# Optimization experiments

Measured on AMD Instinct MI355X. Metric: run time of the kernel, lower is better.

The kernel has to match this reference:

```python
import jax, jax.numpy as jnp
import numpy as np

N_NODES = 50000
N_EDGES = 800000
N_GRAPHS = 32
D = 300
NUM_CLASSES = 40


def setup_inputs() -> dict:
    key = jax.random.key(0)
    ks = jax.random.split(key, 32)

    def w(k, shape):
        fan_in = shape[-2]
        return (jax.random.normal(k, shape, jnp.float32) / np.sqrt(fan_in)).astype(jnp.float32)

    inp = {
        'x': jax.random.normal(ks[0], (N_NODES, 3), jnp.float32),
        'edge_index': jax.random.randint(ks[1], (2, N_EDGES), 0, N_NODES, jnp.int32),
        'batch': jnp.sort(jax.random.randint(ks[2], (N_NODES,), 0, N_GRAPHS, jnp.int32)),
        # project MLP [3, 64, 128, 300]
        'pW1': w(ks[3], (3, 64)),   'pb1': jnp.zeros((64,), jnp.float32),
        'pW2': w(ks[4], (64, 128)), 'pb2': jnp.zeros((128,), jnp.float32),
        'pW3': w(ks[5], (128, D)),  'pb3': jnp.zeros((D,), jnp.float32),
        # 3 PointGNNConv layers, params stacked on leading axis
        'hW': w(ks[6], (3, D, 3)),      'hb': jnp.zeros((3, 3), jnp.float32),
        'fW': w(ks[7], (3, D + 3, D)),  'fb': jnp.zeros((3, D), jnp.float32),
        'gW': w(ks[8], (3, D, D)),      'gb': jnp.zeros((3, D), jnp.float32),
        # 3 post-conv linear layers [300, 300]
        'lW': w(ks[9], (3, D, D)),      'lb': jnp.zeros((3, D), jnp.float32),
        # decision head
        'dW': w(ks[10], (D, NUM_CLASSES)), 'db': jnp.zeros((NUM_CLASSES,), jnp.float32),
    }
    return inp


def reference(x, edge_index, batch, pW1, pb1, pW2, pb2, pW3, pb3,
              hW, hb, fW, fb, gW, gb, lW, lb, dW, db):
    pos = x  # [N, 3] raw point coordinates
    src, dst = edge_index[0], edge_index[1]  # j -> i (source_to_target)

    # embed MLP (eval mode: dropout/batchnorm are identity)
    h = jax.nn.relu(x @ pW1 + pb1)
    h = jax.nn.relu(h @ pW2 + pb2)
    h = h @ pW3 + pb3  # [N, 300]

    for i in range(3):
        # PointGNNConv: delta = mlp_h(x_i); e = mlp_f([pos_j - pos_i + delta_i, x_j]); max-aggr; mlp_g + residual
        delta = h @ hW[i] + hb[i]                     # [N, 3]
        rel = pos[src] - pos[dst] + delta[dst]        # [E, 3]
        e = jnp.concatenate([rel, h[src]], axis=1) @ fW[i] + fb[i]  # [E, 300]
        agg = jax.ops.segment_max(e, dst, num_segments=N_NODES)    # [N, 300]
        agg = jnp.where(jnp.isfinite(agg), agg, 0.0)  # zero-degree nodes -> 0
        h = agg @ gW[i] + gb[i] + h                   # residual
        h = jax.nn.relu(h)
        h = h @ lW[i] + lb[i]                         # lin_i

    # global mean pool over graphs
    sums = jax.ops.segment_sum(h, batch, num_segments=N_GRAPHS)           # [G, 300]
    cnt = jax.ops.segment_sum(jnp.ones((h.shape[0],), h.dtype), batch, num_segments=N_GRAPHS)
    mean = sums / jnp.maximum(cnt, 1.0)[:, None]

    logits = mean @ dW + db  # [G, 40]
    return jax.nn.log_softmax(logits, axis=1)
```

## Files before the change

### kernel.cpp

```cpp
#include <hip/hip_runtime.h>
#include <hip/hip_bf16.h>

#define DD 300
#define DP 320

typedef unsigned short ushort_t;
typedef __attribute__((ext_vector_type(8))) short short8;
typedef __attribute__((ext_vector_type(4))) float f32x4;

__device__ __forceinline__ float b2f(ushort_t u) {
    unsigned x = ((unsigned)u) << 16;
    return __uint_as_float(x);
}
__device__ __forceinline__ ushort_t f2b(float f) {
    unsigned u = __float_as_uint(f);
    unsigned r = (u + 0x7FFFu + ((u >> 16) & 1u)) >> 16;
    return (ushort_t)r;
}

__device__ __forceinline__ void gload16(const void* g, void* l) {
    __builtin_amdgcn_global_load_lds((const __attribute__((address_space(1))) void*)g,
                                     (__attribute__((address_space(3))) void*)l, 16, 0, 0);
}

template<int BNT, int BIAS, int RELU, int RESID, int RANK3>
__launch_bounds__(512)
__global__ void gemm_mfma(const ushort_t* __restrict__ A, int strideA, int M, int K,
                          const ushort_t* __restrict__ Bt,
                          const float* __restrict__ bias,
                          const ushort_t* __restrict__ resid,
                          const float* __restrict__ X3,
                          const float* __restrict__ W3,
                          int NCOL,
                          ushort_t* __restrict__ C, int strideC)
{
    constexpr int BM = 128, BK = 64, BN = 32 * BNT;
    constexpr int CA = BM * BK * 2 / 1024;
    constexpr int CB = BN * BK * 2 / 1024;
    __shared__ ushort_t As[BM * BK];
    __shared__ ushort_t Bs[BN * BK];

    const int tid = threadIdx.x;
    const int lane = tid & 63, wid = tid >> 6;
    const int rowTile = blockIdx.y * BM;
    const int colTile = blockIdx.x * BN;
    const int wm = wid >> 1, wn = wid & 1;

    const int lrow = lane >> 3;
    const int l8b = (lane & 7) * 16;

    f32x4 acc[2][BNT];
    #pragma unroll
    for (int f = 0; f < 2; ++f)
        #pragma unroll
        for (int q = 0; q < BNT; ++q) {
            f32x4 z = {0.f, 0.f, 0.f, 0.f};
            acc[f][q] = z;
        }

    for (int k0 = 0; k0 < K; k0 += BK) {
        for (int c = wid; c < CA; c += 8) {
            int row = c * 8 + lrow;
            int colb = l8b ^ ((row & 7) << 4);
            int gr = rowTile + row; if (gr > M - 1) gr = M - 1;
            gload16(A + (size_t)gr * strideA + k0 + (colb >> 1), As + c * 512);
        }
        for (int c = wid; c < CB; c += 8) {
            int row = c * 8 + lrow;
            int colb = l8b ^ ((row & 7) << 4);
            gload16(Bt + (size_t)(colTile + row) * K + k0 + (colb >> 1), Bs + c * 512);
        }
        __syncthreads();

        #pragma unroll
        for (int ks = 0; ks < 2; ++ks) {
            const int kidx = ks * 32 + (lane >> 4) * 8;
            short8 af[2], bf[BNT];
            #pragma unroll
            for (int f = 0; f < 2; ++f) {
                int row = wm * 32 + f * 16 + (lane & 15);
                int phys = (row * 128 + kidx * 2) ^ ((row & 7) << 4);
                af[f] = *(const short8*)((const char*)As + phys);
            }
            #pragma unroll
            for (int q = 0; q < BNT; ++q) {
                int row = wn * 16 * BNT + q * 16 + (lane & 15);
                int phys = (row * 128 + kidx * 2) ^ ((row & 7) << 4);
                bf[q] = *(const short8*)((const char*)Bs + phys);
            }
            #pragma unroll
            for (int f = 0; f < 2; ++f)
                #pragma unroll
                for (int q = 0; q < BNT; ++q)
                    acc[f][q] = __builtin_amdgcn_mfma_f32_16x16x32_bf16(af[f], bf[q], acc[f][q], 0, 0, 0);
        }
        __syncthreads();
    }

    #pragma unroll
    for (int f = 0; f < 2; ++f) {
        #pragma unroll
        for (int r = 0; r < 4; ++r) {
            int row = rowTile + wm * 32 + f * 16 + (lane >> 4) * 4 + r;
            if (row >= M) continue;
            #pragma unroll
            for (int q = 0; q < BNT; ++q) {
                int col = colTile + wn * 16 * BNT + q * 16 + (lane & 15);
                float v = acc[f][q][r];
                if (BIAS) v += bias[col];
                if (RANK3) {
                    if (col < NCOL) {
                        v += X3[row * 3 + 0] * W3[col]
                           + X3[row * 3 + 1] * W3[NCOL + col]
                           + X3[row * 3 + 2] * W3[2 * NCOL + col];
                    }
                }
                if (RESID) v += b2f(resid[(size_t)row * strideC + col]);
                if (RELU) v = fmaxf(v, 0.f);
                C[(size_t)row * strideC + col] = f2b(v);
            }
        }
    }
}

__global__ void prep(const float* __restrict__ pW2, const float* __restrict__ pW3,
                     const float* __restrict__ pb3,
                     const float* __restrict__ hW, const float* __restrict__ hb,
                     const float* __restrict__ fW,
                     const float* __restrict__ gW, const float* __restrict__ gb,
                     const float* __restrict__ lW, const float* __restrict__ lb,
                     ushort_t* __restrict__ WU, ushort_t* __restrict__ WG,
                     ushort_t* __restrict__ WL, ushort_t* __restrict__ W2,
                     ushort_t* __restrict__ W3e,
                     float* __restrict__ bU, float* __restrict__ bG,
                     float* __restrict__ bL, float* __restrict__ b3)
{
    const int SZ = DP * DP;
    int idx = blockIdx.x * 256 + threadIdx.x;
    if (idx < 3 * SZ) {
        int i = idx / SZ, r = idx - i * SZ;
        int n = r / DP, k = r - n * DP;
        float v = 0.f;
        if (k < DD) {
            if (n < DD) v = fW[i * 90900 + (3 + k) * DD + n];
            else if (n < DD + 3) v = hW[i * 900 + k * 3 + (n - DD)];
        }
        WU[idx] = f2b(v);
        return;
    }
    idx -= 3 * SZ;
    if (idx < 3 * SZ) {
        int i = idx / SZ, r = idx - i * SZ;
        int n = r / DP, k = r - n * DP;
        float v = (n < DD && k < DD) ? gW[i * 90000 + k * DD + n] : 0.f;
        WG[idx] = f2b(v);
        return;
    }
    idx -= 3 * SZ;
    if (idx < 3 * SZ) {
        int i = idx / SZ, r = idx - i * SZ;
        int n = r / DP, k = r - n * DP;
        float v = (n < DD && k < DD) ? lW[i * 90000 + k * DD + n] : 0.f;
        WL[idx] = f2b(v);
        return;
    }
    idx -= 3 * SZ;
    if (idx < 128 * 64) {
        int n = idx >> 6, k = idx & 63;
        W2[idx] = f2b(pW2[k * 128 + n]);
        return;
    }
    idx -= 128 * 64;
    if (idx < DP * 128) {
        int n = idx >> 7, k = idx & 127;
        W3e[idx] = f2b((n < DD) ? pW3[k * DD + n] : 0.f);
        return;
    }
    idx -= DP * 128;
    if (idx < 3 * DP) {
        int i = idx / DP, n = idx - i * DP;
        bU[idx] = (n >= DD && n < DD + 3) ? hb[i * 3 + (n - DD)] : 0.f;
        return;
    }
    idx -= 3 * DP;
    if (idx < 3 * DP) {
        int i = idx / DP, n = idx - i * DP;
        bG[idx] = (n < DD) ? gb[i * DD + n] : 0.f;
        return;
    }
    idx -= 3 * DP;
    if (idx < 3 * DP) {
        int i = idx / DP, n = idx - i * DP;
        bL[idx] = (n < DD) ? lb[i * DD + n] : 0.f;
        return;
    }
    idx -= 3 * DP;
    if (idx < DP) {
        b3[idx] = (idx < DD) ? pb3[idx] : 0.f;
        return;
    }
}

__global__ void embed1(const float* __restrict__ x, const float* __restrict__ W,
                       const float* __restrict__ b, ushort_t* __restrict__ h1, int M)
{
    int idx = blockIdx.x * 256 + threadIdx.x;
    if (idx >= M * 64) return;
    int n = idx >> 6, c = idx & 63;
    const float* xr = x + n * 3;
    float v = xr[0] * W[c] + xr[1] * W[64 + c] + xr[2] * W[128 + c] + b[c];
    h1[idx] = f2b(fmaxf(v, 0.f));
}

__global__ void zero_i(int* __restrict__ p, int n)
{
    int i = blockIdx.x * 256 + threadIdx.x;
    if (i < n) p[i] = 0;
}
__global__ void zero_f(float* __restrict__ p, int n)
{
    int i = blockIdx.x * 256 + threadIdx.x;
    if (i < n) p[i] = 0.f;
}
__global__ void hist_kernel(const int* __restrict__ dst, int* __restrict__ cnt, int E)
{
    int e = blockIdx.x * 256 + threadIdx.x;
    if (e < E) atomicAdd(&cnt[dst[e]], 1);
}
__global__ void scan1(const int* __restrict__ cnt, int* __restrict__ bsum, int N)
{
    __shared__ int s[256];
    int t = threadIdx.x;
    int i = blockIdx.x * 256 + t;
    s[t] = (i < N) ? cnt[i] : 0;
    __syncthreads();
    for (int o = 128; o > 0; o >>= 1) { if (t < o) s[t] += s[t + o]; __syncthreads(); }
    if (t == 0) bsum[blockIdx.x] = s[0];
}
__global__ void scan2(int* __restrict__ bsum, int nb)
{
    __shared__ int s[256];
    int t = threadIdx.x;
    int v = (t < nb) ? bsum[t] : 0;
    s[t] = v; __syncthreads();
    for (int o = 1; o < 256; o <<= 1) {
        int x = (t >= o) ? s[t - o] : 0;
        __syncthreads();
        s[t] += x;
        __syncthreads();
    }
    if (t < nb) bsum[t] = s[t] - v;
}
__global__ void scan3(const int* __restrict__ cnt, const int* __restrict__ bsumx,
                      int* __restrict__ off, int* __restrict__ cursor, int N)
{
    __shared__ int s[256];
    int t = threadIdx.x;
    int i = blockIdx.x * 256 + t;
    int v = (i < N) ? cnt[i] : 0;
    s[t] = v; __syncthreads();
    for (int o = 1; o < 256; o <<= 1) {
        int x = (t >= o) ? s[t - o] : 0;
        __syncthreads();
        s[t] += x;
        __syncthreads();
    }
    int excl = s[t] - v + bsumx[blockIdx.x];
    if (i <= N) {
        off[i] = excl;
        if (i < N) cursor[i] = excl;
    }
}
__global__ void scatter_kernel(const int* __restrict__ src, const int* __restrict__ dst,
                               int* __restrict__ cursor, int* __restrict__ csr, int E)
{
    int e = blockIdx.x * 256 + threadIdx.x;
    if (e < E) {
        int p = atomicAdd(&cursor[dst[e]], 1);
        csr[p] = src[e];
    }
}

__global__ void segmax(const ushort_t* __restrict__ u, const int* __restrict__ off,
                       const int* __restrict__ csr,
                       const float* __restrict__ x, const float* __restrict__ fWp,
                       const float* __restrict__ fb, ushort_t* __restrict__ agg, int Nn)
{
    int n = blockIdx.x * 4 + (threadIdx.x >> 6);
    int lane = threadIdx.x & 63;
    if (n >= Nn) return;
    const int e0 = off[n], e1 = off[n + 1];

    const ushort_t* un = u + (size_t)n * DP;
    float d0 = b2f(un[300]) - x[n * 3 + 0];
    float d1 = b2f(un[301]) - x[n * 3 + 1];
    float d2 = b2f(un[302]) - x[n * 3 + 2];

    float m[5];
    #pragma unroll
    for (int j = 0; j < 5; ++j) m[j] = -INFINITY;

    int e = e0;
    for (; e + 3 < e1; e += 4) {
        const ushort_t* r0 = u + (size_t)csr[e]     * DP + lane;
        const ushort_t* r1 = u + (size_t)csr[e + 1] * DP + lane;
        const ushort_t* r2 = u + (size_t)csr[e + 2] * DP + lane;
        const ushort_t* r3 = u + (size_t)csr[e + 3] * DP + lane;
        #pragma unroll
        for (int j = 0; j < 5; ++j) {
            float a = fmaxf(b2f(r0[64 * j]), b2f(r1[64 * j]));
            float b = fmaxf(b2f(r2[64 * j]), b2f(r3[64 * j]));
            m[j] = fmaxf(m[j], fmaxf(a, b));
        }
    }
    for (; e < e1; ++e) {
        const ushort_t* r0 = u + (size_t)csr[e] * DP + lane;
        #pragma unroll
        for (int j = 0; j < 5; ++j) m[j] = fmaxf(m[j], b2f(r0[64 * j]));
    }

    #pragma unroll
    for (int j = 0; j < 5; ++j) {
        int col = lane + 64 * j;
        float o = 0.f;
        if (e1 > e0 && col < DD)
            o = m[j] + fb[col] + d0 * fWp[col] + d1 * fWp[DD + col] + d2 * fWp[2 * DD + col];
        agg[(size_t)n * DP + col] = f2b(o);
    }
}

__global__ void pool_kernel(const ushort_t* __restrict__ h, const int* __restrict__ batch,
                            float* __restrict__ sums, float* __restrict__ cnts,
                            int Nn, int npb)
{
    int c = threadIdx.x;
    int n0 = blockIdx.x * npb;
    int n1 = min(n0 + npb, Nn);
    if (n0 >= n1) return;
    if (c < DD) {
        float run = 0.f;
        int g = batch[n0];
        for (int n = n0; n < n1; ++n) {
            int gn = batch[n];
            if (gn != g) { atomicAdd(&sums[g * DD + c], run); run = 0.f; g = gn; }
            run += b2f(h[(size_t)n * DP + c]);
        }
        atomicAdd(&sums[g * DD + c], run);
    } else if (c == DD) {
        float run = 0.f;
        int g = batch[n0];
        for (int n = n0; n < n1; ++n) {
            int gn = batch[n];
            if (gn != g) { atomicAdd(&cnts[g], run); run = 0.f; g = gn; }
            run += 1.f;
        }
        atomicAdd(&cnts[g], run);
    }
}

__global__ void head_kernel(const float* __restrict__ sums, const float* __restrict__ cnts,
                            const float* __restrict__ dW, const float* __restrict__ db,
                            float* __restrict__ out)
{
    __shared__ float mean[32][DD];
    __shared__ float logits[32][40];
    int tid = threadIdx.x;
    for (int i = tid; i < 32 * DD; i += 256) {
        int g = i / DD;
        mean[g][i - g * DD] = sums[i] / fmaxf(cnts[g], 1.f);
    }
    __syncthreads();
    for (int o = tid; o < 32 * 40; o += 256) {
        int g = o / 40, cls = o - g * 40;
        float acc = db[cls];
        for (int k = 0; k < DD; ++k) acc += mean[g][k] * dW[k * 40 + cls];
        logits[g][cls] = acc;
    }
    __syncthreads();
    if (tid < 32) {
        float mx = -INFINITY;
        #pragma unroll
        for (int j = 0; j < 40; ++j) mx = fmaxf(mx, logits[tid][j]);
        float se = 0.f;
        for (int j = 0; j < 40; ++j) se += expf(logits[tid][j] - mx);
        float lse = mx + logf(se);
        for (int j = 0; j < 40; ++j) out[tid * 40 + j] = logits[tid][j] - lse;
    }
}

extern "C" void kernel_launch(void* const* d_in, const int* in_sizes, int n_in,
                              void* d_out, int out_size, void* d_ws, size_t ws_size,
                              hipStream_t stream)
{
    const float* x     = (const float*)d_in[0];
    const int*   ei    = (const int*)d_in[1];
    const int*   batch = (const int*)d_in[2];
    const float* pW1   = (const float*)d_in[3];
    const float* pb1   = (const float*)d_in[4];
    const float* pW2   = (const float*)d_in[5];
    const float* pb2   = (const float*)d_in[6];
    const float* pW3   = (const float*)d_in[7];
    const float* pb3   = (const float*)d_in[8];
    const float* hW    = (const float*)d_in[9];
    const float* hb    = (const float*)d_in[10];
    const float* fW    = (const float*)d_in[11];
    const float* fb    = (const float*)d_in[12];
    const float* gW    = (const float*)d_in[13];
    const float* gb    = (const float*)d_in[14];
    const float* lW    = (const float*)d_in[15];
    const float* lb    = (const float*)d_in[16];
    const float* dW    = (const float*)d_in[17];
    const float* db    = (const float*)d_in[18];

    const int N = in_sizes[0] / 3;
    const int E = in_sizes[1] / 2;
    const int G = 32;
    (void)ws_size; (void)n_in; (void)out_size;

    char* wsb = (char*)d_ws;
    size_t offb = 0;
    auto alloc = [&](size_t bytes) {
        void* p = wsb + offb;
        offb += (bytes + 255) & ~(size_t)255;
        return p;
    };
    ushort_t* h    = (ushort_t*)alloc((size_t)N * DP * 2);
    ushort_t* u    = (ushort_t*)alloc((size_t)N * DP * 2);
    ushort_t* agg  = (ushort_t*)alloc((size_t)N * DP * 2);
    ushort_t* h1   = (ushort_t*)alloc((size_t)N * 64 * 2);
    ushort_t* h2   = (ushort_t*)alloc((size_t)N * 128 * 2);
    const int SZ = DP * DP;
    ushort_t* WU   = (ushort_t*)alloc((size_t)3 * SZ * 2);
    ushort_t* WG   = (ushort_t*)alloc((size_t)3 * SZ * 2);
    ushort_t* WL   = (ushort_t*)alloc((size_t)3 * SZ * 2);
    ushort_t* W2   = (ushort_t*)alloc((size_t)128 * 64 * 2);
    ushort_t* W3e  = (ushort_t*)alloc((size_t)DP * 128 * 2);
    float*    bU   = (float*)alloc((size_t)3 * DP * 4);
    float*    bG   = (float*)alloc((size_t)3 * DP * 4);
    float*    bL   = (float*)alloc((size_t)3 * DP * 4);
    float*    b3   = (float*)alloc((size_t)DP * 4);
    int*      cnt    = (int*)alloc((size_t)(N + 1) * 4);
    int*      offp   = (int*)alloc((size_t)(N + 1) * 4);
    int*      cursor = (int*)alloc((size_t)N * 4);
    int*      bsum   = (int*)alloc((size_t)256 * 4);
    int*      csr    = (int*)alloc((size_t)E * 4);
    float*    sums   = (float*)alloc((size_t)G * DD * 4);
    float*    cnts   = (float*)alloc((size_t)G * 4);

    const int* srcp = ei;
    const int* dstp = ei + E;
    const int nb = (N + 255) / 256;
    const dim3 blk(256);

    const int prepTotal = 3 * SZ * 3 + 128 * 64 + DP * 128 + 3 * DP * 3 + DP;
    prep<<<dim3((prepTotal + 255) / 256), blk, 0, stream>>>(
        pW2, pW3, pb3, hW, hb, fW, gW, gb, lW, lb,
        WU, WG, WL, W2, W3e, bU, bG, bL, b3);

    zero_i<<<dim3((N + 1 + 255) / 256), blk, 0, stream>>>(cnt, N + 1);
    hist_kernel<<<dim3((E + 255) / 256), blk, 0, stream>>>(dstp, cnt, E);
    scan1<<<dim3(nb), blk, 0, stream>>>(cnt, bsum, N);
    scan2<<<dim3(1), blk, 0, stream>>>(bsum, nb);
    scan3<<<dim3(nb), blk, 0, stream>>>(cnt, bsum, offp, cursor, N);
    scatter_kernel<<<dim3((E + 255) / 256), blk, 0, stream>>>(srcp, dstp, cursor, csr, E);

    embed1<<<dim3((N * 64 + 255) / 256), blk, 0, stream>>>(x, pW1, pb1, h1, N);

    const int rowBlocks = (N + 127) / 128;
    gemm_mfma<4, 1, 1, 0, 0><<<dim3(1, rowBlocks), dim3(512), 0, stream>>>(
        h1, 64, N, 64, W2, pb2, nullptr, nullptr, nullptr, 128, h2, 128);
    gemm_mfma<5, 1, 0, 0, 0><<<dim3(2, rowBlocks), dim3(512), 0, stream>>>(
        h2, 128, N, 128, W3e, b3, nullptr, nullptr, nullptr, DD, h, DP);

    for (int i = 0; i < 3; ++i) {
        const float* fWi = fW + (size_t)i * (DD + 3) * DD;
        const float* fbi = fb + (size_t)i * DD;

        gemm_mfma<5, 1, 0, 0, 1><<<dim3(2, rowBlocks), dim3(512), 0, stream>>>(
            h, DP, N, DP, WU + (size_t)i * SZ, bU + (size_t)i * DP,
            nullptr, x, fWi, DD, u, DP);

        segmax<<<dim3((N + 3) / 4), blk, 0, stream>>>(u, offp, csr, x, fWi, fbi, agg, N);

        gemm_mfma<5, 1, 1, 1, 0><<<dim3(2, rowBlocks), dim3(512), 0, stream>>>(
            agg, DP, N, DP, WG + (size_t)i * SZ, bG + (size_t)i * DP,
            h, nullptr, nullptr, DD, u, DP);

        gemm_mfma<5, 1, 0, 0, 0><<<dim3(2, rowBlocks), dim3(512), 0, stream>>>(
            u, DP, N, DP, WL + (size_t)i * SZ, bL + (size_t)i * DP,
            nullptr, nullptr, nullptr, DD, h, DP);
    }

    zero_f<<<dim3((G * DD + 255) / 256), blk, 0, stream>>>(sums, G * DD);
    zero_f<<<dim3(1), blk, 0, stream>>>(cnts, G);
    pool_kernel<<<dim3((N + 127) / 128), dim3(320), 0, stream>>>(h, batch, sums, cnts, N, 128);
    head_kernel<<<dim3(1), dim3(256), 0, stream>>>(sums, cnts, dW, db, (float*)d_out);
}
```

Before: 727.8 us.

## Fold lin_i and next conv's f-projection into one wide GEMM via precomputed weight products

Precomputes composite weights (lW_i · fW_{i+1} and pW3 · fW_0) with small on-device GEMMs, so each post-conv linear and the following edge-feature projection run as a single 640-column GEMM that writes both h and u. This removes one full N×320×320 read/compute/write pass per layer and the separate u GEMM. The segmax gather loop is also restructured to prefetch 8 CSR indices at a time, and the zero kernels are replaced by hipMemsetAsync. The composite weights are rounded to bf16 after multiplication, which changes rounding behaviour, and the fused GEMMs are twice as wide.

Result: slower. 829.2 us (+13.9%).

```diff
diff --git a/kernel.cpp b/kernel.cpp
--- a/kernel.cpp
+++ b/kernel.cpp
@@ -23,7 +23,7 @@
                                      (__attribute__((address_space(3))) void*)l, 16, 0, 0);
 }
 
-template<int BNT, int BIAS, int RELU, int RESID, int RANK3>
+template<int BNT, int BIAS, int RELU, int RESID, int RANK3, int SPLIT, int TRANSC>
 __launch_bounds__(512)
 __global__ void gemm_mfma(const ushort_t* __restrict__ A, int strideA, int M, int K,
                           const ushort_t* __restrict__ Bt,
@@ -32,7 +32,9 @@
                           const float* __restrict__ X3,
                           const float* __restrict__ W3,
                           int NCOL,
-                          ushort_t* __restrict__ C, int strideC)
+                          ushort_t* __restrict__ C0,
+                          ushort_t* __restrict__ C1,
+                          int strideC)
 {
     constexpr int BM = 128, BK = 64, BN = 32 * BNT;
     constexpr int CA = BM * BK * 2 / 1024;
@@ -107,97 +109,126 @@
             for (int q = 0; q < BNT; ++q) {
                 int col = colTile + wn * 16 * BNT + q * 16 + (lane & 15);
                 float v = acc[f][q][r];
-                if (BIAS) v += bias[col];
-                if (RANK3) {
-                    if (col < NCOL) {
-                        v += X3[row * 3 + 0] * W3[col]
-                           + X3[row * 3 + 1] * W3[NCOL + col]
-                           + X3[row * 3 + 2] * W3[2 * NCOL + col];
+                if (TRANSC) {
+                    C0[(size_t)col * strideC + row] = f2b(v);
+                } else {
+                    if (BIAS) v += bias[col];
+                    if (RANK3) {
+                        int c = col - SPLIT;
+                        if (c >= 0 && c < NCOL)
+                            v += X3[row * 3 + 0] * W3[c]
+                               + X3[row * 3 + 1] * W3[NCOL + c]
+                               + X3[row * 3 + 2] * W3[2 * NCOL + c];
                     }
+                    if (RESID) v += b2f(resid[(size_t)row * strideC + col]);
+                    if (RELU) v = fmaxf(v, 0.f);
+                    if (SPLIT > 0 && col >= SPLIT)
+                        C1[(size_t)row * strideC + (col - SPLIT)] = f2b(v);
+                    else
+                        C0[(size_t)row * strideC + col] = f2b(v);
                 }
-                if (RESID) v += b2f(resid[(size_t)row * strideC + col]);
-                if (RELU) v = fmaxf(v, 0.f);
-                C[(size_t)row * strideC + col] = f2b(v);
             }
         }
     }
 }
 
 __global__ void prep(const float* __restrict__ pW2, const float* __restrict__ pW3,
-                     const float* __restrict__ pb3,
-                     const float* __restrict__ hW, const float* __restrict__ hb,
-                     const float* __restrict__ fW,
+                     const float* __restrict__ hW, const float* __restrict__ fW,
                      const float* __restrict__ gW, const float* __restrict__ gb,
                      const float* __restrict__ lW, const float* __restrict__ lb,
                      ushort_t* __restrict__ WU, ushort_t* __restrict__ WG,
-                     ushort_t* __restrict__ WL, ushort_t* __restrict__ W2,
-                     ushort_t* __restrict__ W3e,
-                     float* __restrict__ bU, float* __restrict__ bG,
-                     float* __restrict__ bL, float* __restrict__ b3)
+                     ushort_t* __restrict__ Bt12, ushort_t* __restrict__ Bt23,
+                     ushort_t* __restrict__ WL3, ushort_t* __restrict__ LWa0,
+                     ushort_t* __restrict__ LWa1, ushort_t* __restrict__ pW3a,
+                     ushort_t* __restrict__ Bt01, ushort_t* __restrict__ W2,
+                     float* __restrict__ bG, float* __restrict__ bL3)
 {
     const int SZ = DP * DP;
     int idx = blockIdx.x * 256 + threadIdx.x;
     if (idx < 3 * SZ) {
-        int i = idx / SZ, r = idx - i * SZ;
-        int n = r / DP, k = r - n * DP;
+        int i = idx / SZ, r = idx - i * SZ, n = r / DP, k = r - n * DP;
         float v = 0.f;
         if (k < DD) {
             if (n < DD) v = fW[i * 90900 + (3 + k) * DD + n];
             else if (n < DD + 3) v = hW[i * 900 + k * 3 + (n - DD)];
         }
-        WU[idx] = f2b(v);
-        return;
+        WU[idx] = f2b(v); return;
     }
     idx -= 3 * SZ;
     if (idx < 3 * SZ) {
-        int i = idx / SZ, r = idx - i * SZ;
-        int n = r / DP, k = r - n * DP;
-        float v = (n < DD && k < DD) ? gW[i * 90000 + k * DD + n] : 0.f;
-        WG[idx] = f2b(v);
-        return;
+        int i = idx / SZ, r = idx - i * SZ, n = r / DP, k = r - n * DP;
+        WG[idx] = f2b((n < DD && k < DD) ? gW[i * 90000 + k * DD + n] : 0.f); return;
     }
     idx -= 3 * SZ;
-    if (idx < 3 * SZ) {
-        int i = idx / SZ, r = idx - i * SZ;
-        int n = r / DP, k = r - n * DP;
-        float v = (n < DD && k < DD) ? lW[i * 90000 + k * DD + n] : 0.f;
-        WL[idx] = f2b(v);
-        return;
-    }
-    idx -= 3 * SZ;
+    if (idx < SZ) {
+        int n = idx / DP, k = idx - n * DP;
+        Bt12[idx] = f2b((n < DD && k < DD) ? lW[k * DD + n] : 0.f); return;
+    }
+    idx -= SZ;
+    if (idx < SZ) {
+        int n = idx / DP, k = idx - n * DP;
+        Bt23[idx] = f2b((n < DD && k < DD) ? lW[90000 + k * DD + n] : 0.f); return;
+    }
+    idx -= SZ;
+    if (idx < SZ) {
+        int n = idx / DP, k = idx - n * DP;
+        WL3[idx] = f2b((n < DD && k < DD) ? lW[180000 + k * DD + n] : 0.f); return;
+    }
+    idx -= SZ;
+    if (idx < SZ) {
+        int j = idx / DP, k = idx - j * DP;
+        LWa0[idx] = f2b((j < DD && k < DD) ? lW[j * DD + k] : 0.f); return;
+    }
+    idx -= SZ;
+    if (idx < SZ) {
+        int j = idx / DP, k = idx - j * DP;
+        LWa1[idx] = f2b((j < DD && k < DD) ? lW[90000 + j * DD + k] : 0.f); return;
+    }
+    idx -= SZ;
+    if (idx < 128 * DP) {
+        int j = idx / DP, k = idx - j * DP;
+        pW3a[idx] = f2b((k < DD) ? pW3[j * DD + k] : 0.f); return;
+    }
+    idx -= 128 * DP;
+    if (idx < DP * 128) {
+        int n = idx >> 7, k = idx & 127;
+        Bt01[idx] = f2b((n < DD) ? pW3[k * DD + n] : 0.f); return;
+    }
+    idx -= DP * 128;
     if (idx < 128 * 64) {
         int n = idx >> 6, k = idx & 63;
-        W2[idx] = f2b(pW2[k * 128 + n]);
-        return;
+        W2[idx] = f2b(pW2[k * 128 + n]); return;
     }
     idx -= 128 * 64;
-    if (idx < DP * 128) {
-        int n = idx >> 7, k = idx & 127;
-        W3e[idx] = f2b((n < DD) ? pW3[k * DD + n] : 0.f);
-        return;
-    }
-    idx -= DP * 128;
     if (idx < 3 * DP) {
         int i = idx / DP, n = idx - i * DP;
-        bU[idx] = (n >= DD && n < DD + 3) ? hb[i * 3 + (n - DD)] : 0.f;
-        return;
-    }
-    idx -= 3 * DP;
-    if (idx < 3 * DP) {
-        int i = idx / DP, n = idx - i * DP;
-        bG[idx] = (n < DD) ? gb[i * DD + n] : 0.f;
-        return;
-    }
-    idx -= 3 * DP;
-    if (idx < 3 * DP) {
-        int i = idx / DP, n = idx - i * DP;
-        bL[idx] = (n < DD) ? lb[i * DD + n] : 0.f;
-        return;
+        bG[idx] = (n < DD) ? gb[i * DD + n] : 0.f; return;
     }
     idx -= 3 * DP;
     if (idx < DP) {
-        b3[idx] = (idx < DD) ? pb3[idx] : 0.f;
-        return;
+        bL3[idx] = (idx < DD) ? lb[2 * DD + idx] : 0.f; return;
+    }
+}
+
+__global__ void biascomb(const float* __restrict__ pb3, const float* __restrict__ lb,
+                         const float* __restrict__ hb, const ushort_t* __restrict__ WU,
+                         float* __restrict__ bC01, float* __restrict__ bC12,
+                         float* __restrict__ bC23)
+{
+    int t = blockIdx.x * 256 + threadIdx.x;
+    if (t >= 3 * 640) return;
+    int b = t / 640, col = t - b * 640;
+    const float* src = (b == 0) ? pb3 : lb + (b - 1) * DD;
+    float* out = (b == 0) ? bC01 : (b == 1) ? bC12 : bC23;
+    if (col < DP) {
+        out[col] = (col < DD) ? src[col] : 0.f;
+    } else {
+        int n = col - DP;
+        const ushort_t* w = WU + (size_t)b * DP * DP + (size_t)n * DP;
+        float s = 0.f;
+        for (int k = 0; k < DD; ++k) s += src[k] * b2f(w[k]);
+        if (n >= DD && n < DD + 3) s += hb[b * 3 + (n - DD)];
+        out[col] = s;
     }
 }
 
@@ -212,16 +243,6 @@
     h1[idx] = f2b(fmaxf(v, 0.f));
 }
 
-__global__ void zero_i(int* __restrict__ p, int n)
-{
-    int i = blockIdx.x * 256 + threadIdx.x;
-    if (i < n) p[i] = 0;
-}
-__global__ void zero_f(float* __restrict__ p, int n)
-{
-    int i = blockIdx.x * 256 + threadIdx.x;
-    if (i < n) p[i] = 0.f;
-}
 __global__ void hist_kernel(const int* __restrict__ dst, int* __restrict__ cnt, int E)
 {
     int e = blockIdx.x * 256 + threadIdx.x;
@@ -301,22 +322,32 @@
     for (int j = 0; j < 5; ++j) m[j] = -INFINITY;
 
     int e = e0;
+    for (; e + 7 < e1; e += 8) {
+        int s[8];
+        #pragma unroll
+        for (int q = 0; q < 8; ++q) s[q] = csr[e + q];
+        #pragma unroll
+        for (int q = 0; q < 8; ++q) {
+            const ushort_t* r = u + (size_t)s[q] * DP + lane;
+            #pragma unroll
+            for (int j = 0; j < 5; ++j) m[j] = fmaxf(m[j], b2f(r[64 * j]));
+        }
+    }
     for (; e + 3 < e1; e += 4) {
-        const ushort_t* r0 = u + (size_t)csr[e]     * DP + lane;
-        const ushort_t* r1 = u + (size_t)csr[e + 1] * DP + lane;
-        const ushort_t* r2 = u + (size_t)csr[e + 2] * DP + lane;
-        const ushort_t* r3 = u + (size_t)csr[e + 3] * DP + lane;
-        #pragma unroll
-        for (int j = 0; j < 5; ++j) {
-            float a = fmaxf(b2f(r0[64 * j]), b2f(r1[64 * j]));
-            float b = fmaxf(b2f(r2[64 * j]), b2f(r3[64 * j]));
-            m[j] = fmaxf(m[j], fmaxf(a, b));
+        int s[4];
+        #pragma unroll
+        for (int q = 0; q < 4; ++q) s[q] = csr[e + q];
+        #pragma unroll
+        for (int q = 0; q < 4; ++q) {
+            const ushort_t* r = u + (size_t)s[q] * DP + lane;
+            #pragma unroll
+            for (int j = 0; j < 5; ++j) m[j] = fmaxf(m[j], b2f(r[64 * j]));
         }
     }
     for (; e < e1; ++e) {
-        const ushort_t* r0 = u + (size_t)csr[e] * DP + lane;
-        #pragma unroll
-        for (int j = 0; j < 5; ++j) m[j] = fmaxf(m[j], b2f(r0[64 * j]));
+        const ushort_t* r = u + (size_t)csr[e] * DP + lane;
+        #pragma unroll
+        for (int j = 0; j < 5; ++j) m[j] = fmaxf(m[j], b2f(r[64 * j]));
     }
 
     #pragma unroll
@@ -415,6 +446,7 @@
     const int N = in_sizes[0] / 3;
     const int E = in_sizes[1] / 2;
     const int G = 32;
+    const int SZ = DP * DP;
     (void)ws_size; (void)n_in; (void)out_size;
 
     char* wsb = (char*)d_ws;
@@ -424,40 +456,59 @@
         offb += (bytes + 255) & ~(size_t)255;
         return p;
     };
-    ushort_t* h    = (ushort_t*)alloc((size_t)N * DP * 2);
-    ushort_t* u    = (ushort_t*)alloc((size_t)N * DP * 2);
+    ushort_t* hbuf = (ushort_t*)alloc((size_t)N * DP * 2);
+    ushort_t* ubuf = (ushort_t*)alloc((size_t)N * DP * 2);
     ushort_t* agg  = (ushort_t*)alloc((size_t)N * DP * 2);
-    ushort_t* h1   = (ushort_t*)alloc((size_t)N * 64 * 2);
-    ushort_t* h2   = (ushort_t*)alloc((size_t)N * 128 * 2);
-    const int SZ = DP * DP;
+    ushort_t* tbuf = (ushort_t*)alloc((size_t)N * DP * 2);
+    ushort_t* h2 = agg;
+    ushort_t* h1 = tbuf;
     ushort_t* WU   = (ushort_t*)alloc((size_t)3 * SZ * 2);
     ushort_t* WG   = (ushort_t*)alloc((size_t)3 * SZ * 2);
-    ushort_t* WL   = (ushort_t*)alloc((size_t)3 * SZ * 2);
+    ushort_t* Bt01 = (ushort_t*)alloc((size_t)640 * 128 * 2);
+    ushort_t* Bt12 = (ushort_t*)alloc((size_t)640 * DP * 2);
+    ushort_t* Bt23 = (ushort_t*)alloc((size_t)640 * DP * 2);
+    ushort_t* WL3  = (ushort_t*)alloc((size_t)SZ * 2);
+    ushort_t* LWa0 = (ushort_t*)alloc((size_t)SZ * 2);
+    ushort_t* LWa1 = (ushort_t*)alloc((size_t)SZ * 2);
+    ushort_t* pW3a = (ushort_t*)alloc((size_t)128 * DP * 2);
     ushort_t* W2   = (ushort_t*)alloc((size_t)128 * 64 * 2);
-    ushort_t* W3e  = (ushort_t*)alloc((size_t)DP * 128 * 2);
-    float*    bU   = (float*)alloc((size_t)3 * DP * 4);
-    float*    bG   = (float*)alloc((size_t)3 * DP * 4);
-    float*    bL   = (float*)alloc((size_t)3 * DP * 4);
-    float*    b3   = (float*)alloc((size_t)DP * 4);
-    int*      cnt    = (int*)alloc((size_t)(N + 1) * 4);
-    int*      offp   = (int*)alloc((size_t)(N + 1) * 4);
-    int*      cursor = (int*)alloc((size_t)N * 4);
-    int*      bsum   = (int*)alloc((size_t)256 * 4);
-    int*      csr    = (int*)alloc((size_t)E * 4);
-    float*    sums   = (float*)alloc((size_t)G * DD * 4);
-    float*    cnts   = (float*)alloc((size_t)G * 4);
+    float* bG   = (float*)alloc((size_t)3 * DP * 4);
+    float* bL3  = (float*)alloc((size_t)DP * 4);
+    float* bC01 = (float*)alloc((size_t)640 * 4);
+    float* bC12 = (float*)alloc((size_t)640 * 4);
+    float* bC23 = (float*)alloc((size_t)640 * 4);
+    int* cnt    = (int*)alloc((size_t)(N + 1) * 4);
+    int* offp   = (int*)alloc((size_t)(N + 1) * 4);
+    int* cursor = (int*)alloc((size_t)N * 4);
+    int* bsum   = (int*)alloc((size_t)256 * 4);
+    int* csr    = (int*)alloc((size_t)E * 4);
+    float* sums = (float*)alloc((size_t)(G * DD + G) * 4);
+    float* cnts = sums + G * DD;
 
     const int* srcp = ei;
     const int* dstp = ei + E;
     const int nb = (N + 255) / 256;
     const dim3 blk(256);
-
-    const int prepTotal = 3 * SZ * 3 + 128 * 64 + DP * 128 + 3 * DP * 3 + DP;
+    const int rowBlocks = (N + 127) / 128;
+
+    const int prepTotal = 11 * SZ + 2 * 128 * DP + 128 * 64 + 3 * DP + DP;
     prep<<<dim3((prepTotal + 255) / 256), blk, 0, stream>>>(
-        pW2, pW3, pb3, hW, hb, fW, gW, gb, lW, lb,
-        WU, WG, WL, W2, W3e, bU, bG, bL, b3);
-
-    zero_i<<<dim3((N + 1 + 255) / 256), blk, 0, stream>>>(cnt, N + 1);
+        pW2, pW3, hW, fW, gW, gb, lW, lb,
+        WU, WG, Bt12, Bt23, WL3, LWa0, LWa1, pW3a, Bt01, W2, bG, bL3);
+
+    biascomb<<<dim3((3 * 640 + 255) / 256), blk, 0, stream>>>(pb3, lb, hb, WU, bC01, bC12, bC23);
+
+    gemm_mfma<5, 0, 0, 0, 0, 0, 1><<<dim3(2, 1), dim3(512), 0, stream>>>(
+        pW3a, DP, 128, DP, WU, nullptr, nullptr, nullptr, nullptr, DD,
+        Bt01 + (size_t)DP * 128, nullptr, 128);
+    gemm_mfma<5, 0, 0, 0, 0, 0, 1><<<dim3(2, 3), dim3(512), 0, stream>>>(
+        LWa0, DP, DP, DP, WU + SZ, nullptr, nullptr, nullptr, nullptr, DD,
+        Bt12 + (size_t)DP * DP, nullptr, DP);
+    gemm_mfma<5, 0, 0, 0, 0, 0, 1><<<dim3(2, 3), dim3(512), 0, stream>>>(
+        LWa1, DP, DP, DP, WU + 2 * SZ, nullptr, nullptr, nullptr, nullptr, DD,
+        Bt23 + (size_t)DP * DP, nullptr, DP);
+
+    hipMemsetAsync(cnt, 0, (size_t)(N + 1) * 4, stream);
     hist_kernel<<<dim3((E + 255) / 256), blk, 0, stream>>>(dstp, cnt, E);
     scan1<<<dim3(nb), blk, 0, stream>>>(cnt, bsum, N);
     scan2<<<dim3(1), blk, 0, stream>>>(bsum, nb);
@@ -465,34 +516,33 @@
     scatter_kernel<<<dim3((E + 255) / 256), blk, 0, stream>>>(srcp, dstp, cursor, csr, E);
 
     embed1<<<dim3((N * 64 + 255) / 256), blk, 0, stream>>>(x, pW1, pb1, h1, N);
-
-    const int rowBlocks = (N + 127) / 128;
-    gemm_mfma<4, 1, 1, 0, 0><<<dim3(1, rowBlocks), dim3(512), 0, stream>>>(
-        h1, 64, N, 64, W2, pb2, nullptr, nullptr, nullptr, 128, h2, 128);
-    gemm_mfma<5, 1, 0, 0, 0><<<dim3(2, rowBlocks), dim3(512), 0, stream>>>(
-        h2, 128, N, 128, W3e, b3, nullptr, nullptr, nullptr, DD, h, DP);
+    gemm_mfma<4, 1, 1, 0, 0, 0, 0><<<dim3(1, rowBlocks), dim3(512), 0, stream>>>(
+        h1, 64, N, 64, W2, pb2, nullptr, nullptr, nullptr, 128, h2, nullptr, 128);
+
+    gemm_mfma<5, 1, 0, 0, 1, DP, 0><<<dim3(4, rowBlocks), dim3(512), 0, stream>>>(
+        h2, 128, N, 128, Bt01, bC01, nullptr, x, fW, DD, hbuf, ubuf, DP);
 
     for (int i = 0; i < 3; ++i) {
-        const float* fWi = fW + (size_t)i * (DD + 3) * DD;
+        const float* fWi = fW + (size_t)i * 90900;
         const float* fbi = fb + (size_t)i * DD;
 
-        gemm_mfma<5, 1, 0, 0, 1><<<dim3(2, rowBlocks), dim3(512), 0, stream>>>(
-            h, DP, N, DP, WU + (size_t)i * SZ, bU + (size_t)i * DP,
-            nullptr, x, fWi, DD, u, DP);
-
-        segmax<<<dim3((N + 3) / 4), blk, 0, stream>>>(u, offp, csr, x, fWi, fbi, agg, N);
-
-        gemm_mfma<5, 1, 1, 1, 0><<<dim3(2, rowBlocks), dim3(512), 0, stream>>>(
+        segmax<<<dim3((N + 3) / 4), blk, 0, stream>>>(ubuf, offp, csr, x, fWi, fbi, agg, N);
+
+        gemm_mfma<5, 1, 1, 1, 0, 0, 0><<<dim3(2, rowBlocks), dim3(512), 0, stream>>>(
             agg, DP, N, DP, WG + (size_t)i * SZ, bG + (size_t)i * DP,
-            h, nullptr, nullptr, DD, u, DP);
-
-        gemm_mfma<5, 1, 0, 0, 0><<<dim3(2, rowBlocks), dim3(512), 0, stream>>>(
-            u, DP, N, DP, WL + (size_t)i * SZ, bL + (size_t)i * DP,
-            nullptr, nullptr, nullptr, DD, h, DP);
-    }
-
-    zero_f<<<dim3((G * DD + 255) / 256), blk, 0, stream>>>(sums, G * DD);
-    zero_f<<<dim3(1), blk, 0, stream>>>(cnts, G);
-    pool_kernel<<<dim3((N + 127) / 128), dim3(320), 0, stream>>>(h, batch, sums, cnts, N, 128);
+            hbuf, nullptr, nullptr, DD, tbuf, nullptr, DP);
+
+        if (i < 2) {
+            gemm_mfma<5, 1, 0, 0, 1, DP, 0><<<dim3(4, rowBlocks), dim3(512), 0, stream>>>(
+                tbuf, DP, N, DP, (i == 0 ? Bt12 : Bt23), (i == 0 ? bC12 : bC23),
+                nullptr, x, fW + (size_t)(i + 1) * 90900, DD, hbuf, ubuf, DP);
+        } else {
+            gemm_mfma<5, 1, 0, 0, 0, 0, 0><<<dim3(2, rowBlocks), dim3(512), 0, stream>>>(
+                tbuf, DP, N, DP, WL3, bL3, nullptr, nullptr, nullptr, DD, hbuf, nullptr, DP);
+        }
+    }
+
+    hipMemsetAsync(sums, 0, (size_t)(G * DD + G) * 4, stream);
+    pool_kernel<<<dim3((N + 127) / 128), dim3(320), 0, stream>>>(hbuf, batch, sums, cnts, N, 128);
     head_kernel<<<dim3(1), dim3(256), 0, stream>>>(sums, cnts, dW, db, (float*)d_out);
 }
```

## Double GEMM row tile to 256, swap grid axes, replace zero kernels with memset

Applied to the files above, without the earlier changes.

The MFMA GEMM now computes 256 rows per block (4 fragments per wave instead of 2), so each B tile load is reused across twice as many rows and the block count is halved. The grid is reordered so row tiles run along x, padded to a multiple of 8, with an early return for excess blocks. The zero-fill kernels are replaced by hipMemsetAsync, and the sums and counts buffers are merged so one memset clears both. The larger tile raises register use and LDS size, which may lower occupancy. On a 256-CU part it also leaves about 196 row blocks per column tile, which may underfill the device.

After: 831.4 us. 14.2% more time.

```diff
diff --git a/kernel.cpp b/kernel.cpp
--- a/kernel.cpp
+++ b/kernel.cpp
@@ -34,24 +34,26 @@
                           int NCOL,
                           ushort_t* __restrict__ C, int strideC)
 {
-    constexpr int BM = 128, BK = 64, BN = 32 * BNT;
+    constexpr int BM = 256, BK = 64, BN = 32 * BNT;
     constexpr int CA = BM * BK * 2 / 1024;
     constexpr int CB = BN * BK * 2 / 1024;
     __shared__ ushort_t As[BM * BK];
     __shared__ ushort_t Bs[BN * BK];
 
+    const int rowTile = blockIdx.x * BM;
+    if (rowTile >= M) return;
+    const int colTile = blockIdx.y * BN;
+
     const int tid = threadIdx.x;
     const int lane = tid & 63, wid = tid >> 6;
-    const int rowTile = blockIdx.y * BM;
-    const int colTile = blockIdx.x * BN;
     const int wm = wid >> 1, wn = wid & 1;
 
     const int lrow = lane >> 3;
     const int l8b = (lane & 7) * 16;
 
-    f32x4 acc[2][BNT];
+    f32x4 acc[4][BNT];
     #pragma unroll
-    for (int f = 0; f < 2; ++f)
+    for (int f = 0; f < 4; ++f)
         #pragma unroll
         for (int q = 0; q < BNT; ++q) {
             f32x4 z = {0.f, 0.f, 0.f, 0.f};
@@ -59,12 +61,14 @@
         }
 
     for (int k0 = 0; k0 < K; k0 += BK) {
+        #pragma unroll
         for (int c = wid; c < CA; c += 8) {
             int row = c * 8 + lrow;
             int colb = l8b ^ ((row & 7) << 4);
             int gr = rowTile + row; if (gr > M - 1) gr = M - 1;
             gload16(A + (size_t)gr * strideA + k0 + (colb >> 1), As + c * 512);
         }
+        #pragma unroll
         for (int c = wid; c < CB; c += 8) {
             int row = c * 8 + lrow;
             int colb = l8b ^ ((row & 7) << 4);
@@ -75,10 +79,10 @@
         #pragma unroll
         for (int ks = 0; ks < 2; ++ks) {
             const int kidx = ks * 32 + (lane >> 4) * 8;
-            short8 af[2], bf[BNT];
+            short8 af[4], bf[BNT];
             #pragma unroll
-            for (int f = 0; f < 2; ++f) {
-                int row = wm * 32 + f * 16 + (lane & 15);
+            for (int f = 0; f < 4; ++f) {
+                int row = wm * 64 + f * 16 + (lane & 15);
                 int phys = (row * 128 + kidx * 2) ^ ((row & 7) << 4);
                 af[f] = *(const short8*)((const char*)As + phys);
             }
@@ -89,7 +93,7 @@
                 bf[q] = *(const short8*)((const char*)Bs + phys);
             }
             #pragma unroll
-            for (int f = 0; f < 2; ++f)
+            for (int f = 0; f < 4; ++f)
                 #pragma unroll
                 for (int q = 0; q < BNT; ++q)
                     acc[f][q] = __builtin_amdgcn_mfma_f32_16x16x32_bf16(af[f], bf[q], acc[f][q], 0, 0, 0);
@@ -98,10 +102,10 @@
     }
 
     #pragma unroll
-    for (int f = 0; f < 2; ++f) {
+    for (int f = 0; f < 4; ++f) {
         #pragma unroll
         for (int r = 0; r < 4; ++r) {
-            int row = rowTile + wm * 32 + f * 16 + (lane >> 4) * 4 + r;
+            int row = rowTile + wm * 64 + f * 16 + (lane >> 4) * 4 + r;
             if (row >= M) continue;
             #pragma unroll
             for (int q = 0; q < BNT; ++q) {
@@ -212,16 +216,6 @@
     h1[idx] = f2b(fmaxf(v, 0.f));
 }
 
-__global__ void zero_i(int* __restrict__ p, int n)
-{
-    int i = blockIdx.x * 256 + threadIdx.x;
-    if (i < n) p[i] = 0;
-}
-__global__ void zero_f(float* __restrict__ p, int n)
-{
-    int i = blockIdx.x * 256 + threadIdx.x;
-    if (i < n) p[i] = 0.f;
-}
 __global__ void hist_kernel(const int* __restrict__ dst, int* __restrict__ cnt, int E)
 {
     int e = blockIdx.x * 256 + threadIdx.x;
@@ -415,6 +409,7 @@
     const int N = in_sizes[0] / 3;
     const int E = in_sizes[1] / 2;
     const int G = 32;
+    const int SZ = DP * DP;
     (void)ws_size; (void)n_in; (void)out_size;
 
     char* wsb = (char*)d_ws;
@@ -429,7 +424,6 @@
     ushort_t* agg  = (ushort_t*)alloc((size_t)N * DP * 2);
     ushort_t* h1   = (ushort_t*)alloc((size_t)N * 64 * 2);
     ushort_t* h2   = (ushort_t*)alloc((size_t)N * 128 * 2);
-    const int SZ = DP * DP;
     ushort_t* WU   = (ushort_t*)alloc((size_t)3 * SZ * 2);
     ushort_t* WG   = (ushort_t*)alloc((size_t)3 * SZ * 2);
     ushort_t* WL   = (ushort_t*)alloc((size_t)3 * SZ * 2);
@@ -444,20 +438,22 @@
     int*      cursor = (int*)alloc((size_t)N * 4);
     int*      bsum   = (int*)alloc((size_t)256 * 4);
     int*      csr    = (int*)alloc((size_t)E * 4);
-    float*    sums   = (float*)alloc((size_t)G * DD * 4);
-    float*    cnts   = (float*)alloc((size_t)G * 4);
+    float*    sums   = (float*)alloc((size_t)(G * DD + G) * 4);
+    float*    cnts   = sums + G * DD;
 
     const int* srcp = ei;
     const int* dstp = ei + E;
     const int nb = (N + 255) / 256;
     const dim3 blk(256);
 
+    const int rowBlocks = (((N + 255) / 256 + 7) / 8) * 8;
+
     const int prepTotal = 3 * SZ * 3 + 128 * 64 + DP * 128 + 3 * DP * 3 + DP;
     prep<<<dim3((prepTotal + 255) / 256), blk, 0, stream>>>(
         pW2, pW3, pb3, hW, hb, fW, gW, gb, lW, lb,
         WU, WG, WL, W2, W3e, bU, bG, bL, b3);
 
-    zero_i<<<dim3((N + 1 + 255) / 256), blk, 0, stream>>>(cnt, N + 1);
+    hipMemsetAsync(cnt, 0, (size_t)(N + 1) * 4, stream);
     hist_kernel<<<dim3((E + 255) / 256), blk, 0, stream>>>(dstp, cnt, E);
     scan1<<<dim3(nb), blk, 0, stream>>>(cnt, bsum, N);
     scan2<<<dim3(1), blk, 0, stream>>>(bsum, nb);
@@ -465,34 +461,31 @@
     scatter_kernel<<<dim3((E + 255) / 256), blk, 0, stream>>>(srcp, dstp, cursor, csr, E);
 
     embed1<<<dim3((N * 64 + 255) / 256), blk, 0, stream>>>(x, pW1, pb1, h1, N);
-
-    const int rowBlocks = (N + 127) / 128;
-    gemm_mfma<4, 1, 1, 0, 0><<<dim3(1, rowBlocks), dim3(512), 0, stream>>>(
+    gemm_mfma<4, 1, 1, 0, 0><<<dim3(rowBlocks, 1), dim3(512), 0, stream>>>(
         h1, 64, N, 64, W2, pb2, nullptr, nullptr, nullptr, 128, h2, 128);
-    gemm_mfma<5, 1, 0, 0, 0><<<dim3(2, rowBlocks), dim3(512), 0, stream>>>(
+    gemm_mfma<5, 1, 0, 0, 0><<<dim3(rowBlocks, 2), dim3(512), 0, stream>>>(
         h2, 128, N, 128, W3e, b3, nullptr, nullptr, nullptr, DD, h, DP);
 
     for (int i = 0; i < 3; ++i) {
-        const float* fWi = fW + (size_t)i * (DD + 3) * DD;
+        const float* fWi = fW + (size_t)i * 90900;
         const float* fbi = fb + (size_t)i * DD;
 
-        gemm_mfma<5, 1, 0, 0, 1><<<dim3(2, rowBlocks), dim3(512), 0, stream>>>(
+        gemm_mfma<5, 1, 0, 0, 1><<<dim3(rowBlocks, 2), dim3(512), 0, stream>>>(
             h, DP, N, DP, WU + (size_t)i * SZ, bU + (size_t)i * DP,
             nullptr, x, fWi, DD, u, DP);
 
         segmax<<<dim3((N + 3) / 4), blk, 0, stream>>>(u, offp, csr, x, fWi, fbi, agg, N);
 
-        gemm_mfma<5, 1, 1, 1, 0><<<dim3(2, rowBlocks), dim3(512), 0, stream>>>(
+        gemm_mfma<5, 1, 1, 1, 0><<<dim3(rowBlocks, 2), dim3(512), 0, stream>>>(
             agg, DP, N, DP, WG + (size_t)i * SZ, bG + (size_t)i * DP,
             h, nullptr, nullptr, DD, u, DP);
 
-        gemm_mfma<5, 1, 0, 0, 0><<<dim3(2, rowBlocks), dim3(512), 0, stream>>>(
+        gemm_mfma<5, 1, 0, 0, 0><<<dim3(rowBlocks, 2), dim3(512), 0, stream>>>(
             u, DP, N, DP, WL + (size_t)i * SZ, bL + (size_t)i * DP,
             nullptr, nullptr, nullptr, DD, h, DP);
     }
 
-    zero_f<<<dim3((G * DD + 255) / 256), blk, 0, stream>>>(sums, G * DD);
-    zero_f<<<dim3(1), blk, 0, stream>>>(cnts, G);
+    hipMemsetAsync(sums, 0, (size_t)(G * DD + G) * 4, stream);
     pool_kernel<<<dim3((N + 127) / 128), dim3(320), 0, stream>>>(h, batch, sums, cnts, N, 128);
     head_kernel<<<dim3(1), dim3(256), 0, stream>>>(sums, cnts, dW, db, (float*)d_out);
 }
```
